# Performance work log

Hardware: AMD Instinct MI355X
Metric: run time of the kernel (lower is better)

Reference implementation:

```python
import jax, jax.numpy as jnp
import numpy as np

EPS = 1e-5
SLOPE = 0.01  # torch LeakyReLU default


def _leaky(x):
    return jnp.where(x > 0, x, SLOPE * x)


def _layernorm(x, g, b):
    mu = jnp.mean(x, axis=-1, keepdims=True)
    var = jnp.var(x, axis=-1, keepdims=True)
    return (x - mu) * jax.lax.rsqrt(var + EPS) * g + b


def setup_inputs() -> dict:
    key = jax.random.key(0)
    B, N, E, L = 1, 512, 256, 64
    D = E + L  # 320
    ks = jax.random.split(key, 16)
    p = {}
    p["robot_embedding"] = jax.random.normal(ks[0], (B, N, E), jnp.float32)
    p["object_embedding"] = jax.random.normal(ks[1], (B, N, E), jnp.float32)
    p["language_emb"] = jax.random.normal(ks[2], (B, L), jnp.float32)
    # MLPKernel params: Linear(2D->D) + LN + LeakyReLU, Linear(D->D) + LN + LeakyReLU, Linear(D->1)
    p["W1"] = jax.random.normal(ks[3], (2 * D, D), jnp.float32) * 0.02
    p["b1"] = jnp.zeros((D,), jnp.float32)
    p["g1"] = jnp.ones((D,), jnp.float32)
    p["be1"] = jnp.zeros((D,), jnp.float32)
    p["W2"] = jax.random.normal(ks[4], (D, D), jnp.float32) * 0.02
    p["b2"] = jnp.zeros((D,), jnp.float32)
    p["g2"] = jnp.ones((D,), jnp.float32)
    p["be2"] = jnp.zeros((D,), jnp.float32)
    p["W3"] = jax.random.normal(ks[5], (D, 1), jnp.float32) * 0.02
    p["b3"] = jnp.zeros((1,), jnp.float32)
    return p


def _forward(robot_embedding, object_embedding, language_emb,
             W1, b1, g1, be1, W2, b2, g2, be2, W3, b3):
    B, N, E = robot_embedding.shape
    # use_language=True path: z = language_emb, broadcast over N and concat
    z = jnp.broadcast_to(language_emb[:, None, :], (B, N, language_emb.shape[-1]))
    Phi_A = jnp.concatenate([robot_embedding, z], axis=-1)   # [B,N,D]
    Phi_B = jnp.concatenate([object_embedding, z], axis=-1)  # [B,N,D]
    D = Phi_A.shape[-1]
    # Pairwise concat [B,N,N,2D] == kernel(Phi_A_r, Phi_B_r) on the full grid.
    # Equivalent to the block_computing loop (same math, different tiling).
    fA = jnp.broadcast_to(Phi_A[:, :, None, :], (B, N, N, D))
    fB = jnp.broadcast_to(Phi_B[:, None, :, :], (B, N, N, D))
    feat = jnp.concatenate([fA, fB], axis=-1)  # [B,N,N,2D]
    h = _leaky(_layernorm(feat @ W1 + b1, g1, be1))
    h = _leaky(_layernorm(h @ W2 + b2, g2, be2))
    dro = jnp.abs((h @ W3 + b3)[..., 0])  # [B,N,N]
    return dro


def reference(robot_embedding, object_embedding, language_emb,
              W1, b1, g1, be1, W2, b2, g2, be2, W3, b3):
    dro = _forward(robot_embedding, object_embedding, language_emb,
                   W1, b1, g1, be1, W2, b2, g2, be2, W3, b3)
    # outputs = {'dro': dro, 'mu': None, 'logvar': None} -> return dro
    return dro
```

## Files before the change

kernel.cpp:

```cpp
#include <hip/hip_runtime.h>
#include <hip/hip_bf16.h>

#define LN_EPS 1e-5f
#define SLOPE 0.01f

typedef short bf16x8 __attribute__((ext_vector_type(8)));
typedef float f32x4 __attribute__((ext_vector_type(4)));

__global__ __launch_bounds__(320) void prep_kernel(
    const float* __restrict__ robot, const float* __restrict__ object,
    const float* __restrict__ lang, const float* __restrict__ W1,
    const float* __restrict__ b1, const float* __restrict__ W2,
    float* __restrict__ U, float* __restrict__ V,
    __hip_bfloat16* __restrict__ Ub, __hip_bfloat16* __restrict__ VbF,
    float* __restrict__ stats, __hip_bfloat16* __restrict__ W2F)
{
  __shared__ float sh[4][321];
  __shared__ float tile[32][33];
  const int bx = blockIdx.x;
  const int tid = threadIdx.x;

  if (bx < 256) {
    const int i0  = (bx >> 1) * 4;
    const int isV = bx & 1;
    const int d   = tid;
    const float* __restrict__ src   = isV ? object : robot;
    const float* __restrict__ Wbase = W1 + (isV ? 320 * 320 : 0);

    float a0 = 0.f, a1 = 0.f, a2 = 0.f, a3 = 0.f;
#pragma unroll 4
    for (int k = 0; k < 256; ++k) {
      const float w1v = Wbase[k * 320 + d];
      a0 = fmaf(src[(i0 + 0) * 256 + k], w1v, a0);
      a1 = fmaf(src[(i0 + 1) * 256 + k], w1v, a1);
      a2 = fmaf(src[(i0 + 2) * 256 + k], w1v, a2);
      a3 = fmaf(src[(i0 + 3) * 256 + k], w1v, a3);
    }
    float la = 0.f;
#pragma unroll 4
    for (int l = 0; l < 64; ++l)
      la = fmaf(lang[l], Wbase[(256 + l) * 320 + d], la);
    if (isV) la += b1[d];
    a0 += la; a1 += la; a2 += la; a3 += la;

    const float av[4] = {a0, a1, a2, a3};
#pragma unroll
    for (int r = 0; r < 4; ++r) {
      const int i = i0 + r;
      (isV ? V : U)[i * 320 + d] = av[r];
      if (!isV) {
        Ub[i * 320 + d] = __float2bfloat16(av[r]);
      } else {
        const int jt = i >> 4, kkv = d >> 5, gv = (d >> 3) & 3, ev = d & 7;
        VbF[((jt * 10 + kkv) * 512) + (gv * 16 + (i & 15)) * 8 + ev] =
            __float2bfloat16(av[r]);
      }
      sh[r][d] = av[r];
    }
    __syncthreads();
    const int w = tid >> 6, lane = tid & 63;
    if (w < 4) {
      float s = 0.f, q = 0.f;
#pragma unroll
      for (int c = 0; c < 5; ++c) {
        const float v = sh[w][lane + c * 64];
        s += v;
        q = fmaf(v, v, q);
      }
#pragma unroll
      for (int m = 1; m < 64; m <<= 1) {
        s += __shfl_xor(s, m);
        q += __shfl_xor(q, m);
      }
      if (lane == 0) {
        stats[isV * 1024 + i0 + w] = s;
        stats[isV * 1024 + 512 + i0 + w] = q;
      }
    }
  } else {
    const int t = bx - 256;
    const int d0 = (t % 10) * 32;
    const int kk = t / 10;
    if (tid < 256) {
      const int tx = tid & 31, ty = tid >> 5;
#pragma unroll
      for (int r = 0; r < 32; r += 8)
        tile[ty + r][tx] = W2[((kk * 32) + ty + r) * 320 + d0 + tx];
    }
    __syncthreads();
    if (tid < 256) {
      const int fl   = tid >> 7;
      const int l    = (tid >> 1) & 63;
      const int half = tid & 1;
      const int frag = (d0 >> 4) + fl;
      __hip_bfloat16* dst = W2F + ((kk * 20 + frag) * 512) + l * 8 + half * 4;
#pragma unroll
      for (int e = 0; e < 4; ++e)
        dst[e] = __float2bfloat16(tile[(l >> 4) * 8 + half * 4 + e]
                                      [fl * 16 + (l & 15)]);
    }
  }
}

__global__ __launch_bounds__(256, 3) void fused_main(
    const float* __restrict__ U, const float* __restrict__ V,
    const __hip_bfloat16* __restrict__ Ub, const __hip_bfloat16* __restrict__ VbF,
    const __hip_bfloat16* __restrict__ W2F, const float* __restrict__ stats,
    const float* __restrict__ g1, const float* __restrict__ be1,
    const float* __restrict__ b2, const float* __restrict__ g2,
    const float* __restrict__ be2, const float* __restrict__ W3,
    const float* __restrict__ b3, float* __restrict__ out)
{
  __shared__ __align__(16) __hip_bfloat16 h1[64 * 320];
  __shared__ __align__(16) float U_lds[320], g1_lds[320], be1_lds[320];
  __shared__ float dt_lds[64];
  __shared__ float s4[64][5], q4[64][5], e4[64][5];
  __shared__ float rsm[64][2];

  const int i   = blockIdx.x;
  const int j0  = blockIdx.y * 64;
  const int tid = threadIdx.x;
  const int lane = tid & 63;
  const int w    = tid >> 6;
  const int r16  = lane & 15;
  const int g    = lane >> 4;
  const int row  = tid >> 2;
  const int seg  = tid & 3;

  for (int t = tid; t < 320; t += 256) {
    U_lds[t]   = U[i * 320 + t];
    g1_lds[t]  = g1[t];
    be1_lds[t] = be1[t];
  }

  {
    const __hip_bfloat16* __restrict__ Ubrow = Ub + i * 320 + g * 8;
    const __hip_bfloat16* __restrict__ VbFp =
        VbF + ((size_t)((j0 >> 4) + w) * 10) * 512 + lane * 8;
    f32x4 accd = (f32x4){0.f, 0.f, 0.f, 0.f};
#pragma unroll
    for (int kk = 0; kk < 10; ++kk) {
      const bf16x8 da = *(const bf16x8*)(Ubrow + kk * 32);
      const bf16x8 db = *(const bf16x8*)(VbFp + kk * 512);
      accd = __builtin_amdgcn_mfma_f32_16x16x32_bf16(da, db, accd, 0, 0, 0);
    }
    if (lane < 16)
      dt_lds[w * 16 + lane] = accd[0];
  }

  const float* __restrict__ Vrow = V + (j0 + row) * 320 + seg * 80;
  f32x4 vreg[20];
#pragma unroll
  for (int m = 0; m < 20; ++m)
    vreg[m] = *(const f32x4*)(Vrow + m * 4);
  const float sVr = stats[1024 + j0 + row];
  const float qVr = stats[1536 + j0 + row];
  const float sU  = stats[i], qU = stats[512 + i];

  const int wc = w;
  const __hip_bfloat16* __restrict__ Bf = W2F + (size_t)(wc * 5) * 512 + lane * 8;
  bf16x8 bbuf[2][5];
#pragma unroll
  for (int nf = 0; nf < 5; ++nf)
    bbuf[0][nf] = *(const bf16x8*)(Bf + nf * 512);

  __syncthreads();

  const float dt   = dt_lds[row];
  const float mu   = (sU + sVr) * (1.f / 320.f);
  const float var  = (qU + 2.f * dt + qVr) * (1.f / 320.f) - mu * mu;
  const float rs   = rsqrtf(var + LN_EPS);
  const float murs = mu * rs;
  {
    const unsigned swz  = (unsigned)((row & 7) << 4);
    const unsigned base = (unsigned)row * 640u + (unsigned)seg * 160u;
#pragma unroll
    for (int m = 0; m < 10; ++m) {
      const int d = seg * 80 + m * 8;
      const f32x4 va = vreg[2 * m];
      const f32x4 vb = vreg[2 * m + 1];
      const f32x4 ua = *(const f32x4*)&U_lds[d];
      const f32x4 ub = *(const f32x4*)&U_lds[d + 4];
      const f32x4 ga = *(const f32x4*)&g1_lds[d];
      const f32x4 gb = *(const f32x4*)&g1_lds[d + 4];
      const f32x4 ea = *(const f32x4*)&be1_lds[d];
      const f32x4 eb = *(const f32x4*)&be1_lds[d + 4];
      union { bf16x8 v; __hip_bfloat16 e[8]; } pk;
#pragma unroll
      for (int e = 0; e < 4; ++e) {
        const float x = ua[e] + va[e];
        float hv = fmaf(fmaf(x, rs, -murs), ga[e], ea[e]);
        hv = fmaxf(hv, SLOPE * hv);
        pk.e[e] = __float2bfloat16(hv);
      }
#pragma unroll
      for (int e = 0; e < 4; ++e) {
        const float x = ub[e] + vb[e];
        float hv = fmaf(fmaf(x, rs, -murs), gb[e], eb[e]);
        hv = fmaxf(hv, SLOPE * hv);
        pk.e[4 + e] = __float2bfloat16(hv);
      }
      *(bf16x8*)((char*)h1 + ((base + (unsigned)m * 16u) ^ swz)) = pk.v;
    }
  }
  __syncthreads();

  f32x4 acc[4][5];
#pragma unroll
  for (int mf = 0; mf < 4; ++mf)
#pragma unroll
    for (int nf = 0; nf < 5; ++nf)
      acc[mf][nf] = (f32x4){0.f, 0.f, 0.f, 0.f};

  const unsigned swzA = (unsigned)((r16 & 7) << 4);
  unsigned arow[4];
#pragma unroll
  for (int mf = 0; mf < 4; ++mf)
    arow[mf] = (unsigned)(mf * 16 + r16) * 640u;

#pragma unroll
  for (int kk = 0; kk < 10; ++kk) {
    const int cur = kk & 1, nxt = cur ^ 1;
    if (kk < 9) {
#pragma unroll
      for (int nf = 0; nf < 5; ++nf)
        bbuf[nxt][nf] = *(const bf16x8*)(Bf + ((kk + 1) * 20 + nf) * 512);
    }
    const unsigned k2 = (unsigned)((kk * 32 + g * 8) * 2);
    bf16x8 a[4];
#pragma unroll
    for (int mf = 0; mf < 4; ++mf)
      a[mf] = *(const bf16x8*)((const char*)h1 + ((arow[mf] + k2) ^ swzA));
#pragma unroll
    for (int nf = 0; nf < 5; ++nf)
#pragma unroll
      for (int mf = 0; mf < 4; ++mf)
        acc[mf][nf] = __builtin_amdgcn_mfma_f32_16x16x32_bf16(
            a[mf], bbuf[cur][nf], acc[mf][nf], 0, 0, 0);
  }

  float b2c[5], g2c[5], be2c[5], w3c[5];
#pragma unroll
  for (int nf = 0; nf < 5; ++nf) {
    const int col = wc * 80 + nf * 16 + r16;
    b2c[nf]  = b2[col];
    g2c[nf]  = g2[col];
    be2c[nf] = be2[col];
    w3c[nf]  = W3[col];
  }
#pragma unroll
  for (int nf = 0; nf < 5; ++nf)
#pragma unroll
    for (int mf = 0; mf < 4; ++mf)
#pragma unroll
      for (int r = 0; r < 4; ++r)
        acc[mf][nf][r] += b2c[nf];

  float* scr = (float*)h1;
  __syncthreads();

#pragma unroll
  for (int mf = 0; mf < 4; ++mf) {
#pragma unroll
    for (int r = 0; r < 4; ++r) {
      float s = 0.f, q = 0.f;
#pragma unroll
      for (int nf = 0; nf < 5; ++nf) {
        const float v = acc[mf][nf][r];
        s += v;
        q = fmaf(v, v, q);
      }
      const int rw = mf * 16 + g * 4 + r;
      scr[rw * 65 + wc * 16 + r16] = s;
      scr[4160 + rw * 65 + wc * 16 + r16] = q;
    }
  }
  __syncthreads();

  {
    const int r = tid & 63, qq = tid >> 6;
    float s = 0.f, q = 0.f;
#pragma unroll
    for (int k = 0; k < 16; ++k) {
      s += scr[r * 65 + qq * 16 + k];
      q += scr[4160 + r * 65 + qq * 16 + k];
    }
    s4[r][qq] = s;
    q4[r][qq] = q;
  }
  __syncthreads();

  if (tid < 64) {
    const float s = s4[tid][0] + s4[tid][1] + s4[tid][2] + s4[tid][3];
    const float q = q4[tid][0] + q4[tid][1] + q4[tid][2] + q4[tid][3];
    const float mu2  = s * (1.f / 320.f);
    const float var2 = q * (1.f / 320.f) - mu2 * mu2;
    const float rs2  = rsqrtf(var2 + LN_EPS);
    rsm[tid][0] = rs2;
    rsm[tid][1] = mu2 * rs2;
  }
  __syncthreads();

#pragma unroll
  for (int mf = 0; mf < 4; ++mf) {
#pragma unroll
    for (int r = 0; r < 4; ++r) {
      const int rw = mf * 16 + g * 4 + r;
      const float rs2 = rsm[rw][0], murs2 = rsm[rw][1];
      float dsum = 0.f;
#pragma unroll
      for (int nf = 0; nf < 5; ++nf) {
        float v = fmaf(fmaf(acc[mf][nf][r], rs2, -murs2), g2c[nf], be2c[nf]);
        v = fmaxf(v, SLOPE * v);
        dsum = fmaf(v, w3c[nf], dsum);
      }
      scr[rw * 65 + wc * 16 + r16] = dsum;
    }
  }
  __syncthreads();

  {
    const int r = tid & 63, qq = tid >> 6;
    float s = 0.f;
#pragma unroll
    for (int k = 0; k < 16; ++k)
      s += scr[r * 65 + qq * 16 + k];
    e4[r][qq] = s;
  }
  __syncthreads();

  if (tid < 64) {
    const float tot = e4[tid][0] + e4[tid][1] + e4[tid][2] + e4[tid][3] + b3[0];
    out[i * 512 + j0 + tid] = fabsf(tot);
  }
}

extern "C" void kernel_launch(void* const* d_in, const int* in_sizes, int n_in,
                              void* d_out, int out_size, void* d_ws, size_t ws_size,
                              hipStream_t stream) {
  const float* robot  = (const float*)d_in[0];
  const float* object = (const float*)d_in[1];
  const float* lang   = (const float*)d_in[2];
  const float* W1  = (const float*)d_in[3];
  const float* b1  = (const float*)d_in[4];
  const float* g1  = (const float*)d_in[5];
  const float* be1 = (const float*)d_in[6];
  const float* W2  = (const float*)d_in[7];
  const float* b2  = (const float*)d_in[8];
  const float* g2  = (const float*)d_in[9];
  const float* be2 = (const float*)d_in[10];
  const float* W3  = (const float*)d_in[11];
  const float* b3  = (const float*)d_in[12];
  float* out = (float*)d_out;

  float* U     = (float*)d_ws;
  float* V     = U + 512 * 320;
  float* stats = V + 512 * 320;
  __hip_bfloat16* W2F = (__hip_bfloat16*)(stats + 2048);
  __hip_bfloat16* Ub  = W2F + 320 * 320;
  __hip_bfloat16* VbF = Ub + 512 * 320;

  prep_kernel<<<356, 320, 0, stream>>>(robot, object, lang, W1, b1, W2,
                                       U, V, Ub, VbF, stats, W2F);
  fused_main<<<dim3(512, 8), 256, 0, stream>>>(U, V, Ub, VbF, W2F, stats,
                                               g1, be1, b2, g2, be2, W3, b3,
                                               out);
}
```

Measured before the change: 193.2 us.

## Split prep into bf16 conversion kernel and MFMA GEMM for U/V projections

Replaces the scalar fp32 FMA projection of robot/object embeddings through W1 with a conversion kernel, which builds bf16 concatenated inputs and fragment-packed W1 and W2, followed by a bf16 MFMA GEMM kernel. The GEMM also produces U/V, their bf16 layouts and the LayerNorm row stats. The aim is to cut prep-stage cost by using matrix cores instead of per-thread scalar loops. It adds an extra kernel launch, only 16 blocks for the GEMM, and bf16 rounding of the first-layer projection inputs, which lowers precision.

```diff
diff --git a/kernel.cpp b/kernel.cpp
--- a/kernel.cpp
+++ b/kernel.cpp
@@ -7,98 +7,199 @@
 typedef short bf16x8 __attribute__((ext_vector_type(8)));
 typedef float f32x4 __attribute__((ext_vector_type(4)));
 
-__global__ __launch_bounds__(320) void prep_kernel(
+__global__ __launch_bounds__(256) void convert_kernel(
     const float* __restrict__ robot, const float* __restrict__ object,
     const float* __restrict__ lang, const float* __restrict__ W1,
-    const float* __restrict__ b1, const float* __restrict__ W2,
-    float* __restrict__ U, float* __restrict__ V,
-    __hip_bfloat16* __restrict__ Ub, __hip_bfloat16* __restrict__ VbF,
-    float* __restrict__ stats, __hip_bfloat16* __restrict__ W2F)
+    const float* __restrict__ W2,
+    __hip_bfloat16* __restrict__ AcatU, __hip_bfloat16* __restrict__ AcatV,
+    __hip_bfloat16* __restrict__ W1Ft, __hip_bfloat16* __restrict__ W1Fb,
+    __hip_bfloat16* __restrict__ W2F)
 {
-  __shared__ float sh[4][321];
   __shared__ float tile[32][33];
   const int bx = blockIdx.x;
   const int tid = threadIdx.x;
 
-  if (bx < 256) {
-    const int i0  = (bx >> 1) * 4;
-    const int isV = bx & 1;
-    const int d   = tid;
-    const float* __restrict__ src   = isV ? object : robot;
-    const float* __restrict__ Wbase = W1 + (isV ? 320 * 320 : 0);
-
-    float a0 = 0.f, a1 = 0.f, a2 = 0.f, a3 = 0.f;
-#pragma unroll 4
-    for (int k = 0; k < 256; ++k) {
-      const float w1v = Wbase[k * 320 + d];
-      a0 = fmaf(src[(i0 + 0) * 256 + k], w1v, a0);
-      a1 = fmaf(src[(i0 + 1) * 256 + k], w1v, a1);
-      a2 = fmaf(src[(i0 + 2) * 256 + k], w1v, a2);
-      a3 = fmaf(src[(i0 + 3) * 256 + k], w1v, a3);
-    }
-    float la = 0.f;
-#pragma unroll 4
-    for (int l = 0; l < 64; ++l)
-      la = fmaf(lang[l], Wbase[(256 + l) * 320 + d], la);
-    if (isV) la += b1[d];
-    a0 += la; a1 += la; a2 += la; a3 += la;
-
-    const float av[4] = {a0, a1, a2, a3};
+  if (bx < 300) {
+    int kk, d0;
+    const float* srcbase;
+    __hip_bfloat16* dstbase;
+    if (bx < 200) {
+      kk = bx / 10; d0 = (bx % 10) * 32;
+      srcbase = W1 + (size_t)(kk * 32) * 320;
+      dstbase = (kk < 10) ? W1Ft : W1Fb;
+      if (kk >= 10) kk -= 10;
+    } else {
+      const int t = bx - 200;
+      kk = t / 10; d0 = (t % 10) * 32;
+      srcbase = W2 + (size_t)(kk * 32) * 320;
+      dstbase = W2F;
+    }
+    const int tx = tid & 31, ty = tid >> 5;
+#pragma unroll
+    for (int r = 0; r < 32; r += 8)
+      tile[ty + r][tx] = srcbase[(ty + r) * 320 + d0 + tx];
+    __syncthreads();
+    const int fl   = tid >> 7;
+    const int l    = (tid >> 1) & 63;
+    const int half = tid & 1;
+    const int frag = (d0 >> 4) + fl;
+    __hip_bfloat16* dst = dstbase + ((kk * 20 + frag) * 512) + l * 8 + half * 4;
+#pragma unroll
+    for (int e = 0; e < 4; ++e)
+      dst[e] = __float2bfloat16(tile[(l >> 4) * 8 + half * 4 + e]
+                                    [fl * 16 + (l & 15)]);
+  } else {
+    const int i0 = (bx - 300) * 2;
+#pragma unroll
+    for (int rr = 0; rr < 2; ++rr) {
+      const int i = i0 + rr;
+      AcatU[i * 320 + tid] = __float2bfloat16(robot[i * 256 + tid]);
+      AcatV[i * 320 + tid] = __float2bfloat16(object[i * 256 + tid]);
+      if (tid < 64) {
+        const __hip_bfloat16 lv = __float2bfloat16(lang[tid]);
+        AcatU[i * 320 + 256 + tid] = lv;
+        AcatV[i * 320 + 256 + tid] = lv;
+      }
+    }
+  }
+}
+
+__global__ __launch_bounds__(256, 3) void prep_gemm(
+    const __hip_bfloat16* __restrict__ AcatU,
+    const __hip_bfloat16* __restrict__ AcatV,
+    const __hip_bfloat16* __restrict__ W1Ft,
+    const __hip_bfloat16* __restrict__ W1Fb,
+    const float* __restrict__ b1,
+    float* __restrict__ U, float* __restrict__ V,
+    __hip_bfloat16* __restrict__ Ub, __hip_bfloat16* __restrict__ VbF,
+    float* __restrict__ stats)
+{
+  __shared__ __align__(16) __hip_bfloat16 hA[64 * 320];
+  __shared__ float s4[64][5], q4[64][5];
+
+  const int it = blockIdx.x, uv = blockIdx.y;
+  const int i0 = it * 64;
+  const int tid = threadIdx.x;
+  const int lane = tid & 63;
+  const int w    = tid >> 6;
+  const int r16  = lane & 15;
+  const int g    = lane >> 4;
+  const int row  = tid >> 2;
+  const int seg  = tid & 3;
+
+  const __hip_bfloat16* __restrict__ Acat = uv ? AcatV : AcatU;
+  const __hip_bfloat16* __restrict__ W1F  = uv ? W1Fb : W1Ft;
+
+  {
+    const __hip_bfloat16* __restrict__ src =
+        Acat + (size_t)(i0 + row) * 320 + seg * 80;
+    const unsigned swz  = (unsigned)((row & 7) << 4);
+    const unsigned base = (unsigned)row * 640u + (unsigned)seg * 160u;
+#pragma unroll
+    for (int m = 0; m < 10; ++m) {
+      const bf16x8 v = *(const bf16x8*)(src + m * 8);
+      *(bf16x8*)((char*)hA + ((base + (unsigned)m * 16u) ^ swz)) = v;
+    }
+  }
+
+  const int wc = w;
+  const __hip_bfloat16* __restrict__ Bf = W1F + (size_t)(wc * 5) * 512 + lane * 8;
+  bf16x8 bbuf[2][5];
+#pragma unroll
+  for (int nf = 0; nf < 5; ++nf)
+    bbuf[0][nf] = *(const bf16x8*)(Bf + nf * 512);
+
+  __syncthreads();
+
+  f32x4 acc[4][5];
+#pragma unroll
+  for (int mf = 0; mf < 4; ++mf)
+#pragma unroll
+    for (int nf = 0; nf < 5; ++nf)
+      acc[mf][nf] = (f32x4){0.f, 0.f, 0.f, 0.f};
+
+  const unsigned swzA = (unsigned)((r16 & 7) << 4);
+  unsigned arow[4];
+#pragma unroll
+  for (int mf = 0; mf < 4; ++mf)
+    arow[mf] = (unsigned)(mf * 16 + r16) * 640u;
+
+#pragma unroll
+  for (int kk = 0; kk < 10; ++kk) {
+    const int cur = kk & 1, nxt = cur ^ 1;
+    if (kk < 9) {
+#pragma unroll
+      for (int nf = 0; nf < 5; ++nf)
+        bbuf[nxt][nf] = *(const bf16x8*)(Bf + ((kk + 1) * 20 + nf) * 512);
+    }
+    const unsigned k2 = (unsigned)((kk * 32 + g * 8) * 2);
+    bf16x8 a[4];
+#pragma unroll
+    for (int mf = 0; mf < 4; ++mf)
+      a[mf] = *(const bf16x8*)((const char*)hA + ((arow[mf] + k2) ^ swzA));
+#pragma unroll
+    for (int nf = 0; nf < 5; ++nf)
+#pragma unroll
+      for (int mf = 0; mf < 4; ++mf)
+        acc[mf][nf] = __builtin_amdgcn_mfma_f32_16x16x32_bf16(
+            a[mf], bbuf[cur][nf], acc[mf][nf], 0, 0, 0);
+  }
+
+  float b1c[5];
+#pragma unroll
+  for (int nf = 0; nf < 5; ++nf)
+    b1c[nf] = uv ? b1[wc * 80 + nf * 16 + r16] : 0.f;
+
+  float* scr = (float*)hA;
+  __syncthreads();
+
+#pragma unroll
+  for (int mf = 0; mf < 4; ++mf) {
 #pragma unroll
     for (int r = 0; r < 4; ++r) {
-      const int i = i0 + r;
-      (isV ? V : U)[i * 320 + d] = av[r];
-      if (!isV) {
-        Ub[i * 320 + d] = __float2bfloat16(av[r]);
-      } else {
-        const int jt = i >> 4, kkv = d >> 5, gv = (d >> 3) & 3, ev = d & 7;
-        VbF[((jt * 10 + kkv) * 512) + (gv * 16 + (i & 15)) * 8 + ev] =
-            __float2bfloat16(av[r]);
-      }
-      sh[r][d] = av[r];
-    }
-    __syncthreads();
-    const int w = tid >> 6, lane = tid & 63;
-    if (w < 4) {
+      const int j = i0 + mf * 16 + g * 4 + r;
       float s = 0.f, q = 0.f;
 #pragma unroll
-      for (int c = 0; c < 5; ++c) {
-        const float v = sh[w][lane + c * 64];
-        s += v;
-        q = fmaf(v, v, q);
-      }
-#pragma unroll
-      for (int m = 1; m < 64; m <<= 1) {
-        s += __shfl_xor(s, m);
-        q += __shfl_xor(q, m);
-      }
-      if (lane == 0) {
-        stats[isV * 1024 + i0 + w] = s;
-        stats[isV * 1024 + 512 + i0 + w] = q;
-      }
-    }
-  } else {
-    const int t = bx - 256;
-    const int d0 = (t % 10) * 32;
-    const int kk = t / 10;
-    if (tid < 256) {
-      const int tx = tid & 31, ty = tid >> 5;
-#pragma unroll
-      for (int r = 0; r < 32; r += 8)
-        tile[ty + r][tx] = W2[((kk * 32) + ty + r) * 320 + d0 + tx];
-    }
-    __syncthreads();
-    if (tid < 256) {
-      const int fl   = tid >> 7;
-      const int l    = (tid >> 1) & 63;
-      const int half = tid & 1;
-      const int frag = (d0 >> 4) + fl;
-      __hip_bfloat16* dst = W2F + ((kk * 20 + frag) * 512) + l * 8 + half * 4;
-#pragma unroll
-      for (int e = 0; e < 4; ++e)
-        dst[e] = __float2bfloat16(tile[(l >> 4) * 8 + half * 4 + e]
-                                      [fl * 16 + (l & 15)]);
-    }
+      for (int nf = 0; nf < 5; ++nf) {
+        const float val = acc[mf][nf][r] + b1c[nf];
+        const int d = wc * 80 + nf * 16 + r16;
+        if (uv == 0) {
+          U[j * 320 + d] = val;
+          Ub[j * 320 + d] = __float2bfloat16(val);
+        } else {
+          V[j * 320 + d] = val;
+          VbF[((size_t)(j >> 4) * 10 + (d >> 5)) * 512 +
+              (((d >> 3) & 3) * 16 + (j & 15)) * 8 + (d & 7)] =
+              __float2bfloat16(val);
+        }
+        s += val;
+        q = fmaf(val, val, q);
+      }
+      const int rw = mf * 16 + g * 4 + r;
+      scr[rw * 65 + wc * 16 + r16] = s;
+      scr[4160 + rw * 65 + wc * 16 + r16] = q;
+    }
+  }
+  __syncthreads();
+
+  {
+    const int r = tid & 63, qq = tid >> 6;
+    float s = 0.f, q = 0.f;
+#pragma unroll
+    for (int k = 0; k < 16; ++k) {
+      s += scr[r * 65 + qq * 16 + k];
+      q += scr[4160 + r * 65 + qq * 16 + k];
+    }
+    s4[r][qq] = s;
+    q4[r][qq] = q;
+  }
+  __syncthreads();
+
+  if (tid < 64) {
+    const float s = s4[tid][0] + s4[tid][1] + s4[tid][2] + s4[tid][3];
+    const float q = q4[tid][0] + q4[tid][1] + q4[tid][2] + q4[tid][3];
+    stats[uv * 1024 + i0 + tid] = s;
+    stats[uv * 1024 + 512 + i0 + tid] = q;
   }
 }
 
@@ -356,12 +457,18 @@
   float* U     = (float*)d_ws;
   float* V     = U + 512 * 320;
   float* stats = V + 512 * 320;
-  __hip_bfloat16* W2F = (__hip_bfloat16*)(stats + 2048);
-  __hip_bfloat16* Ub  = W2F + 320 * 320;
-  __hip_bfloat16* VbF = Ub + 512 * 320;
-
-  prep_kernel<<<356, 320, 0, stream>>>(robot, object, lang, W1, b1, W2,
-                                       U, V, Ub, VbF, stats, W2F);
+  __hip_bfloat16* W2F   = (__hip_bfloat16*)(stats + 2048);
+  __hip_bfloat16* Ub    = W2F + 320 * 320;
+  __hip_bfloat16* VbF   = Ub + 512 * 320;
+  __hip_bfloat16* AcatU = VbF + 512 * 320;
+  __hip_bfloat16* AcatV = AcatU + 512 * 320;
+  __hip_bfloat16* W1Ft  = AcatV + 512 * 320;
+  __hip_bfloat16* W1Fb  = W1Ft + 320 * 320;
+
+  convert_kernel<<<556, 256, 0, stream>>>(robot, object, lang, W1, W2,
+                                          AcatU, AcatV, W1Ft, W1Fb, W2F);
+  prep_gemm<<<dim3(8, 2), 256, 0, stream>>>(AcatU, AcatV, W1Ft, W1Fb, b1,
+                                            U, V, Ub, VbF, stats);
   fused_main<<<dim3(512, 8), 256, 0, stream>>>(U, V, Ub, VbF, W2F, stats,
                                                g1, be1, b2, g2, be2, W3, b3,
                                                out);
```

New measurement: 182.3 us. 1.06x faster.
